# Kernel tuning notes

Measured on AMD Instinct MI355X. Metric: run time of the kernel, lower is better.

Reference implementation:

```python
import jax, jax.numpy as jnp
import numpy as np

TAU = 2.0      # LIF membrane time constant
EPS = 1e-5     # BatchNorm eps
HEADS = 8
SCALE = 0.125
ALPHA = 4.0    # surrogate sigmoid sharpness

@jax.custom_vjp
def spike(x):
    return (x >= 0.0).astype(x.dtype)

def _spike_fwd(x):
    return spike(x), x

def _spike_bwd(x, g):
    s = jax.nn.sigmoid(ALPHA * x)
    return (g * ALPHA * s * (1.0 - s),)

spike.defvjp(_spike_fwd, _spike_bwd)

def lif(x_seq, v_th):
    # multi-step LIF, v_reset=0, hard reset; x_seq: [T, ...]
    def step(v, x):
        v = v + (x - v) / TAU
        s = spike(v - v_th)
        v = (1.0 - s) * v  # hard reset to 0
        return v, s
    v0 = jnp.zeros_like(x_seq[0])
    _, spikes = jax.lax.scan(step, v0, x_seq)
    return spikes

def bn(x, gamma, beta, mean, var):
    # inference-mode BatchNorm1d over channel axis; x: [T,B,C,N], params: [C]
    inv = gamma * jax.lax.rsqrt(var + EPS)
    return x * inv[:, None] + (beta - mean * inv)[:, None]

def setup_inputs() -> dict:
    key = jax.random.key(0)
    k1, k2 = jax.random.split(key)
    T, B, C, N, H = 4, 64, 512, 196, HEADS
    x = jax.random.normal(k1, (T, B, C, N), dtype=jnp.float32)
    res_attn = jnp.zeros((T, B, H, N, N), dtype=jnp.float32)
    w = jax.random.normal(k2, (4, C, C), dtype=jnp.float32) / np.sqrt(C)
    bn_gamma = jnp.ones((4, C), dtype=jnp.float32)
    bn_beta = jnp.zeros((4, C), dtype=jnp.float32)
    bn_mean = jnp.zeros((4, C), dtype=jnp.float32)
    bn_var = jnp.ones((4, C), dtype=jnp.float32)
    return {"x": x, "res_attn": res_attn, "w": w, "bn_gamma": bn_gamma,
            "bn_beta": bn_beta, "bn_mean": bn_mean, "bn_var": bn_var}

def reference(x, res_attn, w, bn_gamma, bn_beta, bn_mean, bn_var):
    T, B, C, N = x.shape
    H = HEADS
    D = C // H

    def qkv_branch(i):
        y = jnp.einsum('oc,tbcn->tbon', w[i], x)          # conv1x1
        y = bn(y, bn_gamma[i], bn_beta[i], bn_mean[i], bn_var[i])
        return lif(y, 1.0)                                # binary spikes

    def to_heads(t):  # [T,B,C,N] -> [T,B,H,N,D]
        return t.transpose(0, 1, 3, 2).reshape(T, B, N, H, D).transpose(0, 1, 3, 2, 4)

    q = to_heads(qkv_branch(0))
    k = to_heads(qkv_branch(1))
    v = to_heads(qkv_branch(2))

    attn = jnp.einsum('tbhnd,tbhmd->tbhnm', q, k) * SCALE
    o = jnp.einsum('tbhnm,tbhmd->tbhnd', attn, v)
    o = o.transpose(0, 1, 2, 4, 3).reshape(T, B, C, N)    # [T,B,H,D,N] -> [T,B,C,N]
    o = lif(o, 0.5)                                       # attn_lif, v_threshold=0.5
    o = jnp.einsum('oc,tbcn->tbon', w[3], o)              # proj conv1x1
    o = bn(o, bn_gamma[3], bn_beta[3], bn_mean[3], bn_var[3])
    o = lif(o, 1.0)                                       # proj_lif
    return (o, attn)
```

## Files before the change

### kernel.cpp

```cpp
#include <hip/hip_runtime.h>
#include <stdint.h>
#include <math.h>

#define T_ 4
#define B_ 64
#define C_ 512
#define N_ 196
#define H_ 8
#define OE_ 25690112ull
#define TBHN (T_*B_*H_*N_)

using u16 = unsigned short;
using u32 = unsigned int;
using u64 = unsigned long long;
using u8  = unsigned char;

typedef __attribute__((ext_vector_type(8))) short bf16x8;
typedef __attribute__((ext_vector_type(4))) float f32x4;
typedef const float __attribute__((address_space(4))) cfloat_as4;

typedef const void __attribute__((address_space(1))) gvoid;
typedef void __attribute__((address_space(3))) svoid;

__device__ __forceinline__ void gld_lds4(const void* g, void* l){
  __builtin_amdgcn_global_load_lds((gvoid*)g, (svoid*)l, 4, 0, 0);
}

__device__ __forceinline__ float b2f(u16 u){
  union { u32 i; float f; } x; x.i = ((u32)u) << 16; return x.f;
}
__device__ __forceinline__ u16 f2b(float f){
  union { float g; u32 i; } x; x.g = f; return (u16)(x.i >> 16);
}
__device__ __forceinline__ float ldf(const void* p, size_t i, bool f32){
  return f32 ? ((const float*)p)[i] : b2f(((const u16*)p)[i]);
}
__device__ __forceinline__ bool is_f32(const void* var){
  return ((const u32*)var)[0] == 0x3F800000u;
}

__global__ __launch_bounds__(256) void transpose_w(
    const void* __restrict__ w, float* __restrict__ wT, const void* __restrict__ var)
{
  const bool f32 = is_f32(var);
  __shared__ float tile[32][33];
  const int br = blockIdx.z;
  const int c0 = blockIdx.x*32, o0 = blockIdx.y*32;
  const int tx = threadIdx.x & 31, ty = threadIdx.x >> 5;
  const size_t base = (size_t)br*C_*C_;
  #pragma unroll
  for (int r = 0; r < 32; r += 8)
    tile[ty+r][tx] = ldf(w, base + (size_t)(o0+ty+r)*C_ + (c0+tx), f32);
  __syncthreads();
  #pragma unroll
  for (int r = 0; r < 32; r += 8)
    wT[base + (size_t)(c0+ty+r)*C_ + (o0+tx)] = tile[tx][ty+r];
}

template<int DT>
__device__ __forceinline__ void conv_main(
    const void* __restrict__ xin, const float* __restrict__ wp,
    u8* __restrict__ xsraw, const int wv, const int lane, const int fl0,
    float acc[4][8])
{
  const size_t cn   = (size_t)C_*N_;
  const size_t tstr = (size_t)B_*cn;

  int e0;
  if (DT == 0)      e0 = lane;
  else if (DT == 1) e0 = 2*(lane & 31);
  else              e0 = 4*(lane & 15);
  const int fl = fl0 + e0;
  const int b  = fl / N_;
  const int n  = fl - b*N_;
  const size_t lbase = (size_t)wv*tstr + (size_t)b*cn + (size_t)n;

  auto issue = [&](int k){
    const int buf = k & 1;
    const int rb  = (buf*4 + wv)*8;
    if (DT == 2){
      const u8* bp = (const u8*)xin + lbase;
      #pragma unroll
      for (int g = 0; g < 2; g++){
        const int cl = g*4 + (lane >> 4);
        gld_lds4(bp + (size_t)(k*8 + cl)*N_, xsraw + (size_t)(rb + g*4)*64);
      }
    } else if (DT == 0){
      const float* bp = (const float*)xin + lbase;
      #pragma unroll
      for (int cl = 0; cl < 8; cl++){
        gld_lds4(bp + (size_t)(k*8 + cl)*N_, xsraw + (size_t)(rb + cl)*256);
      }
    } else {
      const u16* bp = (const u16*)xin + lbase;
      #pragma unroll
      for (int p = 0; p < 4; p++){
        const int cl = p*2 + (lane >> 5);
        gld_lds4(bp + (size_t)(k*8 + cl)*N_, xsraw + (size_t)(rb + p*2)*128);
      }
    }
  };

  issue(0);
  for (int k = 0; k < 64; k++){
    __syncthreads();
    if (k + 1 < 64) issue(k + 1);
    const int buf = k & 1;
    #pragma unroll
    for (int cc = 0; cc < 8; cc++){
      const int c = (k << 3) + cc;
      float xv[4];
      #pragma unroll
      for (int t = 0; t < 4; t++){
        const int ei = ((buf*4 + t)*8 + cc)*64 + lane;
        if (DT == 2)      xv[t] = (float)xsraw[ei];
        else if (DT == 0) xv[t] = ((const float*)xsraw)[ei];
        else              xv[t] = b2f(((const u16*)xsraw)[ei]);
      }
      cfloat_as4* wr = (cfloat_as4*)(uintptr_t)(wp + (size_t)c*C_);
      #pragma unroll
      for (int j = 0; j < 8; j++){
        const float ww = wr[j];
        #pragma unroll
        for (int t = 0; t < 4; t++) acc[t][j] = fmaf(ww, xv[t], acc[t][j]);
      }
    }
  }
}

template<int IN_U8, int OUT_MODE>
__global__ __launch_bounds__(256, 4) void conv_gld(
    const void* __restrict__ xin, const float* __restrict__ wT,
    const void* __restrict__ gamma, const void* __restrict__ beta,
    const void* __restrict__ mean,  const void* __restrict__ var,
    int br, float vth, void* __restrict__ outp)
{
  __shared__ __align__(16) u8 xsraw[16384];
  __shared__ u32 P[4*64];
  const bool f32 = is_f32(var);
  const int tid  = threadIdx.x;
  const int lane = tid & 63;
  const int wv   = tid >> 6;
  const int cb   = blockIdx.y;
  const int co0  = __builtin_amdgcn_readfirstlane(cb*32 + wv*8);
  const int fl0  = blockIdx.x*64;
  const int fl   = fl0 + lane;
  const int b    = fl / N_;
  const int n    = fl - b*N_;

  if (OUT_MODE == 0){ P[tid] = 0; }

  float acc[4][8];
  #pragma unroll
  for (int t=0;t<4;t++)
    #pragma unroll
    for (int j=0;j<8;j++) acc[t][j] = 0.f;

  const float* __restrict__ wp = wT + (size_t)br*C_*C_ + co0;

  if (IN_U8)    conv_main<2>(xin, wp, xsraw, wv, lane, fl0, acc);
  else if (f32) conv_main<0>(xin, wp, xsraw, wv, lane, fl0, acc);
  else          conv_main<1>(xin, wp, xsraw, wv, lane, fl0, acc);

  {
    #pragma clang fp contract(off)
    u32 m8[4] = {0,0,0,0};
    #pragma unroll
    for (int j=0;j<8;j++){
      const int co = co0 + j;
      const size_t pb = (size_t)br*C_ + co;
      const float gf  = ldf(gamma, pb, f32);
      const float bef = ldf(beta,  pb, f32);
      const float mnf = ldf(mean,  pb, f32);
      const float vrf = ldf(var,   pb, f32);
      const float rs   = 1.0f / sqrtf(vrf + 1e-5f);
      const float invf = gf * rs;
      const float mi   = mnf * invf;
      const float shf  = bef - mi;
      float vm = 0.f;
      #pragma unroll
      for (int t=0;t<4;t++){
        float xy = acc[t][j] * invf;
        float x  = xy + shf;
        float d  = x - vm;
        float v  = vm + d * 0.5f;
        bool  s  = (v >= vth);
        vm = s ? 0.f : v;
        if (OUT_MODE == 0){
          m8[t] |= (s ? 1u : 0u) << j;
        } else {
          size_t off = ((size_t)(t*B_ + b)*C_ + co)*(size_t)N_ + n;
          if (OUT_MODE == 1){
            ((u8*)outp)[off] = s ? 1 : 0;
          } else {
            if (f32) ((float*)outp)[off] = s ? 1.f : 0.f;
            else     ((u16*)outp)[off]   = s ? (u16)0x3F80 : (u16)0;
          }
        }
      }
    }
    if (OUT_MODE == 0){
      #pragma unroll
      for (int t=0;t<4;t++)
        atomicOr(&P[t*64 + lane], m8[t] << (wv*8));
    }
  }
  if (OUT_MODE == 0){
    __syncthreads();
    const int t2 = tid >> 6, l2 = tid & 63;
    const int f2 = blockIdx.x*64 + l2;
    const int b2 = f2 / N_, n2 = f2 - b2*N_;
    const int h2 = cb >> 1, half = cb & 1;
    ((u32*)outp)[(((size_t)(t2*B_ + b2)*H_ + h2)*N_ + n2)*2 + half] = P[tid];
  }
}

__global__ __launch_bounds__(256) void qk_popc(
    const u64* __restrict__ q64, const u64* __restrict__ k64,
    void* __restrict__ outp, const void* __restrict__ var)
{
  const bool f32 = is_f32(var);
  __shared__ u64 qs[8];
  const int n0  = blockIdx.x * 8;
  const int tbh = blockIdx.y;
  const int tid = threadIdx.x;
  if (tid < 8){
    int n = n0 + tid;
    qs[tid] = (n < N_) ? q64[(size_t)tbh*N_ + n] : 0ull;
  }
  __syncthreads();
  const u64* krow = k64 + (size_t)tbh*N_;
  const size_t abase = OE_ + (size_t)tbh*(size_t)(N_*N_);
  #pragma unroll
  for (int kk = 0; kk < 4; kk++){
    int lin = kk*256 + tid;
    if (lin < 8*98){
      int rn = lin / 98;
      int mp = lin - rn*98;
      int n  = n0 + rn;
      if (n < N_){
        u64 qv = qs[rn];
        float c0 = (float)__popcll(qv & krow[2*mp    ]) * 0.125f;
        float c1 = (float)__popcll(qv & krow[2*mp + 1]) * 0.125f;
        size_t e = abase + (size_t)n*N_ + 2*mp;
        if (f32){
          ((float*)outp)[e]   = c0;
          ((float*)outp)[e+1] = c1;
        } else {
          u32 pk = (u32)f2b(c0) | ((u32)f2b(c1) << 16);
          *(u32*)((u16*)outp + e) = pk;
        }
      }
    }
  }
}

__global__ __launch_bounds__(256) void attnv_mfma(
    const void* __restrict__ outp ,
    const u8* __restrict__ sv, u8* __restrict__ s3,
    const void* __restrict__ var)
{
  const bool f32 = is_f32(var);
  __shared__ __align__(16) u16 Vt[64*232];
  __shared__ __align__(16) u16 At[16*232];
  const int nt  = blockIdx.x;
  const int gy  = blockIdx.y;
  const int h   = gy & 7, b = gy >> 3;
  const int tid = threadIdx.x;
  const int lane = tid & 63;
  const int mrow = lane & 15, quad = lane >> 4;
  const int d0  = (tid >> 6) * 16;
  const int n0  = nt * 16;
  const bool wvalid = (nt < 12) || (quad == 0);
  float vmem[4] = {0.f, 0.f, 0.f, 0.f};

  for (int t = 0; t < 4; t++){
    const size_t tb = (size_t)t*B_ + b;
    __syncthreads();
    {
      const u8* vb = sv + (tb*C_ + (size_t)h*64)*(size_t)N_;
      for (int i = tid; i < 64*56; i += 256){
        int r = i / 56, wd = i - r*56;
        u32 b4 = (wd < 49) ? *(const u32*)(vb + (size_t)r*N_ + wd*4) : 0u;
        short4 o4;
        o4.x = (b4 & 0xffu)       ? (short)0x3F80 : (short)0;
        o4.y = (b4 & 0xff00u)     ? (short)0x3F80 : (short)0;
        o4.z = (b4 & 0xff0000u)   ? (short)0x3F80 : (short)0;
        o4.w = (b4 & 0xff000000u) ? (short)0x3F80 : (short)0;
        *(short4*)(Vt + r*232 + wd*4) = o4;
      }
    }
    {
      const size_t ab = OE_ + ((tb*H_ + h)*(size_t)N_)*(size_t)N_;
      for (int i = tid; i < 16*224; i += 256){
        int r = i / 224, m = i - r*224;
        int n = n0 + r;
        float a = 0.f;
        if (n < N_ && m < N_) a = ldf(outp, ab + (size_t)n*N_ + m, f32) * 8.0f;
        At[r*232 + m] = f2b(a);
      }
    }
    __syncthreads();
    f32x4 acc = {0.f, 0.f, 0.f, 0.f};
    #pragma unroll
    for (int k = 0; k < 7; k++){
      bf16x8 av = *(const bf16x8*)(At + mrow*232        + k*32 + quad*8);
      bf16x8 bv = *(const bf16x8*)(Vt + (d0+mrow)*232   + k*32 + quad*8);
      acc = __builtin_amdgcn_mfma_f32_16x16x32_bf16(av, bv, acc, 0, 0, 0);
    }
    {
      #pragma clang fp contract(off)
      u32 pk = 0;
      #pragma unroll
      for (int r = 0; r < 4; r++){
        float o  = acc[r] * 0.125f;
        float dd = o - vmem[r];
        float v  = vmem[r] + dd * 0.5f;
        bool  s  = (v >= 0.5f);
        vmem[r] = s ? 0.f : v;
        pk |= (s ? 1u : 0u) << (8*r);
      }
      if (wvalid){
        const int d = d0 + mrow;
        *(u32*)(s3 + (tb*C_ + (size_t)h*64 + d)*(size_t)N_ + n0 + quad*4) = pk;
      }
    }
  }
}

extern "C" void kernel_launch(void* const* d_in, const int* in_sizes, int n_in,
                              void* d_out, int out_size, void* d_ws, size_t ws_size,
                              hipStream_t stream)
{
  (void)in_sizes; (void)n_in; (void)out_size; (void)ws_size;
  const void* x     = d_in[0];
  const void* w     = d_in[2];
  const void* gamma = d_in[3];
  const void* beta  = d_in[4];
  const void* mean  = d_in[5];
  const void* var   = d_in[6];

  u8*  sv  = (u8*)d_ws;
  u8*  s3  = sv + OE_;
  u64* q64 = (u64*)(s3 + OE_);
  u64* k64 = q64 + TBHN;
  float* wT = (float*)(k64 + TBHN);

  transpose_w<<<dim3(16,16,4), 256, 0, stream>>>(w, wT, var);

  dim3 cgrid(196, 16);
  conv_gld<0,0><<<cgrid, 256, 0, stream>>>(x, wT, gamma, beta, mean, var, 0, 1.0f, (void*)q64);
  conv_gld<0,0><<<cgrid, 256, 0, stream>>>(x, wT, gamma, beta, mean, var, 1, 1.0f, (void*)k64);
  conv_gld<0,1><<<cgrid, 256, 0, stream>>>(x, wT, gamma, beta, mean, var, 2, 1.0f, (void*)sv);

  qk_popc<<<dim3(25, T_*B_*H_), 256, 0, stream>>>(q64, k64, d_out, var);

  attnv_mfma<<<dim3(13, B_*H_), 256, 0, stream>>>(d_out, sv, s3, var);

  conv_gld<1,2><<<cgrid, 256, 0, stream>>>((const void*)s3, wT, gamma, beta, mean, var, 3, 1.0f, d_out);
}
```

Measured before the change: 2.434 ms.

## Fuse QK popcount attention into attn-V MFMA kernel and keep V as bytes in LDS

Merges the separate popcount QK kernel into the attention-times-V kernel. Each block now computes its 16-row attention tile directly from packed q/k bits, writes it to the output, and feeds it to the MFMA without reading the attention matrix back from global memory. V spikes are staged in LDS as raw bytes and expanded to bf16 in registers just before each MFMA, which halves LDS footprint. The cost is more in-kernel ALU work and one fewer launch; the large attention write remains.

```diff
diff --git a/kernel.cpp b/kernel.cpp
--- a/kernel.cpp
+++ b/kernel.cpp
@@ -215,53 +215,14 @@
   }
 }
 
-__global__ __launch_bounds__(256) void qk_popc(
+__global__ __launch_bounds__(256) void attnqk_mfma(
     const u64* __restrict__ q64, const u64* __restrict__ k64,
-    void* __restrict__ outp, const void* __restrict__ var)
-{
-  const bool f32 = is_f32(var);
-  __shared__ u64 qs[8];
-  const int n0  = blockIdx.x * 8;
-  const int tbh = blockIdx.y;
-  const int tid = threadIdx.x;
-  if (tid < 8){
-    int n = n0 + tid;
-    qs[tid] = (n < N_) ? q64[(size_t)tbh*N_ + n] : 0ull;
-  }
-  __syncthreads();
-  const u64* krow = k64 + (size_t)tbh*N_;
-  const size_t abase = OE_ + (size_t)tbh*(size_t)(N_*N_);
-  #pragma unroll
-  for (int kk = 0; kk < 4; kk++){
-    int lin = kk*256 + tid;
-    if (lin < 8*98){
-      int rn = lin / 98;
-      int mp = lin - rn*98;
-      int n  = n0 + rn;
-      if (n < N_){
-        u64 qv = qs[rn];
-        float c0 = (float)__popcll(qv & krow[2*mp    ]) * 0.125f;
-        float c1 = (float)__popcll(qv & krow[2*mp + 1]) * 0.125f;
-        size_t e = abase + (size_t)n*N_ + 2*mp;
-        if (f32){
-          ((float*)outp)[e]   = c0;
-          ((float*)outp)[e+1] = c1;
-        } else {
-          u32 pk = (u32)f2b(c0) | ((u32)f2b(c1) << 16);
-          *(u32*)((u16*)outp + e) = pk;
-        }
-      }
-    }
-  }
-}
-
-__global__ __launch_bounds__(256) void attnv_mfma(
-    const void* __restrict__ outp ,
+    void* __restrict__ outp ,
     const u8* __restrict__ sv, u8* __restrict__ s3,
     const void* __restrict__ var)
 {
   const bool f32 = is_f32(var);
-  __shared__ __align__(16) u16 Vt[64*232];
+  __shared__ __align__(16) u8  Vu[64*232];
   __shared__ __align__(16) u16 At[16*232];
   const int nt  = blockIdx.x;
   const int gy  = blockIdx.y;
@@ -275,38 +236,63 @@
   float vmem[4] = {0.f, 0.f, 0.f, 0.f};
 
   for (int t = 0; t < 4; t++){
-    const size_t tb = (size_t)t*B_ + b;
+    const size_t tb  = (size_t)t*B_ + b;
+    const size_t tbh = tb*H_ + h;
     __syncthreads();
     {
-      const u8* vb = sv + (tb*C_ + (size_t)h*64)*(size_t)N_;
-      for (int i = tid; i < 64*56; i += 256){
-        int r = i / 56, wd = i - r*56;
-        u32 b4 = (wd < 49) ? *(const u32*)(vb + (size_t)r*N_ + wd*4) : 0u;
-        short4 o4;
-        o4.x = (b4 & 0xffu)       ? (short)0x3F80 : (short)0;
-        o4.y = (b4 & 0xff00u)     ? (short)0x3F80 : (short)0;
-        o4.z = (b4 & 0xff0000u)   ? (short)0x3F80 : (short)0;
-        o4.w = (b4 & 0xff000000u) ? (short)0x3F80 : (short)0;
-        *(short4*)(Vt + r*232 + wd*4) = o4;
+      const u32* vb = (const u32*)(sv + (tb*C_ + (size_t)h*64)*(size_t)N_);
+      #pragma unroll
+      for (int it = 0; it < 15; it++){
+        int i = it*256 + tid;
+        if (i < 64*58){
+          int r = i / 58, wd = i - r*58;
+          u32 v = (wd < 49) ? vb[r*49 + wd] : 0u;
+          *(u32*)(Vu + r*232 + wd*4) = v;
+        }
       }
     }
     {
-      const size_t ab = OE_ + ((tb*H_ + h)*(size_t)N_)*(size_t)N_;
-      for (int i = tid; i < 16*224; i += 256){
-        int r = i / 224, m = i - r*224;
+      const u64* kr = k64 + tbh*(size_t)N_;
+      const u64* qr = q64 + tbh*(size_t)N_;
+      const size_t abase = OE_ + tbh*(size_t)(N_*N_);
+      #pragma unroll
+      for (int it = 0; it < 7; it++){
+        int i = it*256 + tid;
+        int r = i / 112, mp = i - r*112;
         int n = n0 + r;
-        float a = 0.f;
-        if (n < N_ && m < N_) a = ldf(outp, ab + (size_t)n*N_ + m, f32) * 8.0f;
-        At[r*232 + m] = f2b(a);
+        int m0 = mp*2;
+        u64 qv = (n < N_) ? qr[n] : 0ull;
+        u64 kk0 = (m0 < N_)     ? kr[m0]     : 0ull;
+        u64 kk1 = (m0 + 1 < N_) ? kr[m0 + 1] : 0ull;
+        float c0 = (float)__popcll(qv & kk0);
+        float c1 = (float)__popcll(qv & kk1);
+        *(u32*)(At + r*232 + m0) = (u32)f2b(c0) | ((u32)f2b(c1) << 16);
+        if (n < N_ && m0 < N_){
+          size_t e = abase + (size_t)n*N_ + m0;
+          if (f32){
+            float2 st; st.x = c0*0.125f; st.y = c1*0.125f;
+            *(float2*)((float*)outp + e) = st;
+          } else {
+            *(u32*)((u16*)outp + e) =
+                (u32)f2b(c0*0.125f) | ((u32)f2b(c1*0.125f) << 16);
+          }
+        }
       }
     }
     __syncthreads();
     f32x4 acc = {0.f, 0.f, 0.f, 0.f};
     #pragma unroll
     for (int k = 0; k < 7; k++){
-      bf16x8 av = *(const bf16x8*)(At + mrow*232        + k*32 + quad*8);
-      bf16x8 bv = *(const bf16x8*)(Vt + (d0+mrow)*232   + k*32 + quad*8);
-      acc = __builtin_amdgcn_mfma_f32_16x16x32_bf16(av, bv, acc, 0, 0, 0);
+      bf16x8 av = *(const bf16x8*)(At + mrow*232 + k*32 + quad*8);
+      u64 vx = *(const u64*)(Vu + (d0+mrow)*232 + k*32 + quad*8);
+      u32 x0 = (u32)vx, x1 = (u32)(vx >> 32);
+      u32 o0 = (x0 & 1u)*0x3F80u         + (x0 & 0x100u)*0x3F8000u;
+      u32 o1 = ((x0 >> 16) & 1u)*0x3F80u + ((x0 >> 16) & 0x100u)*0x3F8000u;
+      u32 o2 = (x1 & 1u)*0x3F80u         + (x1 & 0x100u)*0x3F8000u;
+      u32 o3 = ((x1 >> 16) & 1u)*0x3F80u + ((x1 >> 16) & 0x100u)*0x3F8000u;
+      union { u32 w[4]; bf16x8 v; } bu;
+      bu.w[0] = o0; bu.w[1] = o1; bu.w[2] = o2; bu.w[3] = o3;
+      acc = __builtin_amdgcn_mfma_f32_16x16x32_bf16(av, bu.v, acc, 0, 0, 0);
     }
     {
       #pragma clang fp contract(off)
@@ -353,9 +339,7 @@
   conv_gld<0,0><<<cgrid, 256, 0, stream>>>(x, wT, gamma, beta, mean, var, 1, 1.0f, (void*)k64);
   conv_gld<0,1><<<cgrid, 256, 0, stream>>>(x, wT, gamma, beta, mean, var, 2, 1.0f, (void*)sv);
 
-  qk_popc<<<dim3(25, T_*B_*H_), 256, 0, stream>>>(q64, k64, d_out, var);
-
-  attnv_mfma<<<dim3(13, B_*H_), 256, 0, stream>>>(d_out, sv, s3, var);
+  attnqk_mfma<<<dim3(13, B_*H_), 256, 0, stream>>>(q64, k64, d_out, sv, s3, var);
 
   conv_gld<1,2><<<cgrid, 256, 0, stream>>>((const void*)s3, wT, gamma, beta, mean, var, 3, 1.0f, d_out);
 }
```

Measured after the change: 2.269 ms. 1.07x faster.
